# Optimization experiments

Hardware: AMD Instinct MI355X
Metric: run time of the kernel (lower is better)

## Reference

```python
import jax, jax.numpy as jnp
import numpy as np

SEQ_LEN, BATCH, VOCAB, EMB, HID, LAYERS = 128, 64, 10000, 1024, 1024, 2

def setup_inputs() -> dict:
    key = jax.random.key(0)
    ks = jax.random.split(key, 8)
    inputs = jax.random.randint(ks[0], (SEQ_LEN, BATCH), 0, VOCAB)
    hidden = jnp.zeros((LAYERS, BATCH, HID), jnp.float32)
    # parameters (uniform init like the torch module)
    emb = jax.random.uniform(ks[1], (VOCAB, EMB), jnp.float32, -0.1, 0.1)
    # per-layer RNN cell params (emb_size == hidden_size so Wx stacks uniformly)
    s = 1.0 / np.sqrt(HID)
    Wx = jax.random.uniform(ks[2], (LAYERS, HID, HID), jnp.float32, -s, s)
    Wh = jax.random.uniform(ks[3], (LAYERS, HID, HID), jnp.float32, -s, s)
    b = jax.random.uniform(ks[4], (LAYERS, HID), jnp.float32, -s, s)
    fcW = jax.random.uniform(ks[5], (VOCAB, HID), jnp.float32, -0.1, 0.1)
    fcb = jnp.zeros((VOCAB,), jnp.float32)
    return {"inputs": inputs, "hidden": hidden, "emb": emb, "Wx": Wx,
            "Wh": Wh, "b": b, "fcW": fcW, "fcb": fcb}

def reference(inputs, hidden, emb, Wx, Wh, b, fcW, fcb):
    num_layers = hidden.shape[0]

    def step(h, tok):
        x = emb[tok]  # [B, EMB] embedding lookup (dropout = identity, keep_prob=1)
        new_h = []
        for j in range(num_layers):  # small static loop over layers
            hj = jnp.tanh(x @ Wx[j] + h[j] @ Wh[j] + b[j])  # [B, H]
            new_h.append(hj)
            x = hj
        logits = x @ fcW.T + fcb  # [B, V]
        return jnp.stack(new_h), logits

    h_final, logits = jax.lax.scan(step, hidden, inputs)
    return logits, h_final  # [S,B,V], [L,B,H]
```

## Files before the change

### kernel.cpp

```cpp
#include <hip/hip_runtime.h>
#include <hip/hip_bf16.h>
#include <math.h>

typedef __hip_bfloat16 bf16;
typedef __attribute__((ext_vector_type(8))) short short8;
typedef __attribute__((ext_vector_type(4))) float floatx4;

#define SEQ   128
#define BATCH 64
#define VOCAB 10000
#define HID   1024
#define TAIL  81920000
#define PNL   131072

#define MFMA(a,b,c) __builtin_amdgcn_mfma_f32_16x16x32_bf16((a),(b),(c),0,0,0)

#define LDA_U64(p)   __hip_atomic_load((const unsigned long long*)(p), __ATOMIC_RELAXED, __HIP_MEMORY_SCOPE_AGENT)
#define LDAQ_I32(p)  __hip_atomic_load((const int*)(p), __ATOMIC_ACQUIRE, __HIP_MEMORY_SCOPE_AGENT)
#define STA_U32(p,v) __hip_atomic_store((unsigned int*)(p), (v), __ATOMIC_RELAXED, __HIP_MEMORY_SCOPE_AGENT)
#define ADDR_I32(p)  __hip_atomic_fetch_add((int*)(p), 1, __ATOMIC_RELEASE, __HIP_MEMORY_SCOPE_AGENT)

union U16B { unsigned long long u[2]; short8 s; };

__device__ inline unsigned int pack2(float lo, float hi) {
  unsigned short a = __builtin_bit_cast(unsigned short, __float2bfloat16(lo));
  unsigned short b = __builtin_bit_cast(unsigned short, __float2bfloat16(hi));
  return ((unsigned int)b << 16) | (unsigned int)a;
}

__device__ inline void gl_lds16(const bf16* g, bf16* s) {
  __builtin_amdgcn_global_load_lds(
      (const __attribute__((address_space(1))) void*)g,
      (__attribute__((address_space(3))) void*)s, 16, 0, 0);
}

__device__ inline float ld_in(const void* p, size_t i, int f) {
  return f ? ((const float*)p)[i] : __bfloat162float(((const bf16*)p)[i]);
}

__global__ __launch_bounds__(256) void detect(const unsigned short* __restrict__ u,
                                              int* __restrict__ flag) {
  __shared__ int smax;
  if (threadIdx.x == 0) smax = 0;
  __syncthreads();
  int mymax = 0;
  for (int i = threadIdx.x * 2; i < 4096; i += 512) {
    int e = (u[i] >> 7) & 0xFF;
    mymax = max(mymax, e);
  }
  atomicMax(&smax, mymax);
  __syncthreads();
  if (threadIdx.x == 0) {
    flag[0] = (smax >= 0xF0) ? 1 : 0;
    flag[1] = 0;
    flag[2] = 0;
  }
}

__global__ __launch_bounds__(256) void convert_any(const void* __restrict__ src,
                                                   bf16* __restrict__ dst, int n,
                                                   const int* __restrict__ flagp) {
  int f = *flagp;
  for (int i = blockIdx.x * 256 + threadIdx.x; i < n; i += gridDim.x * 256)
    dst[i] = __float2bfloat16(ld_in(src, (size_t)i, f));
}

__global__ __launch_bounds__(256) void init_hidden(const void* __restrict__ src,
                                                   bf16* __restrict__ h0,
                                                   bf16* __restrict__ h1,
                                                   const int* __restrict__ flagp) {
  int f = *flagp;
  int i = blockIdx.x * 256 + threadIdx.x;
  if (i < 65536) {
    h0[i] = __float2bfloat16(ld_in(src, (size_t)i, f));
    h1[i] = __float2bfloat16(ld_in(src, (size_t)(65536 + i), f));
  }
}

__global__ __launch_bounds__(256) void transpose4(const void* __restrict__ Wx,
                                                  const void* __restrict__ Wh,
                                                  bf16* __restrict__ Wt,
                                                  const int* __restrict__ flagp) {
  __shared__ bf16 tile[64][65];
  int f = *flagp;
  int z = blockIdx.z;
  const void* src = (z & 1) ? Wh : Wx;
  size_t loff = (z >> 1) ? (size_t)HID * HID : 0;
  bf16* dst = Wt + (size_t)z * HID * HID;
  int r0 = blockIdx.x * 64, c0 = blockIdx.y * 64;
  int t = threadIdx.x, cc = t & 63, rg = t >> 6;
  #pragma unroll
  for (int i = 0; i < 16; ++i) {
    int r = rg * 16 + i;
    tile[r][cc] = __float2bfloat16(ld_in(src, loff + (size_t)(r0 + r) * HID + c0 + cc, f));
  }
  __syncthreads();
  #pragma unroll
  for (int i = 0; i < 16; ++i) {
    int j = rg * 16 + i;
    dst[(size_t)(c0 + j) * HID + r0 + cc] = tile[cc][j];
  }
}

__global__ __launch_bounds__(256) void gemm_a0(
    const int*  __restrict__ tok,
    const bf16* __restrict__ emb,
    const bf16* __restrict__ Wx0t,
    const bf16* __restrict__ b0,
    float* __restrict__ A0)
{
  __shared__ __align__(16) bf16 sA[128 * 32];
  __shared__ __align__(16) bf16 sB[128 * 32];
  int m0 = blockIdx.x * 128, n0 = blockIdx.y * 128;
  int t = threadIdx.x, lane = t & 63, w = t >> 6;
  int wm = (w >> 1) * 64, wn = (w & 1) * 64;
  int quad = lane >> 4, l16 = lane & 15;

  int r0 = t >> 2, kc = t & 3;
  const bf16* ga0 = emb + (size_t)tok[m0 + r0] * HID + kc * 8;
  const bf16* ga1 = emb + (size_t)tok[m0 + r0 + 64] * HID + kc * 8;
  const bf16* gb0 = Wx0t + (size_t)(n0 + r0) * HID + kc * 8;
  const bf16* gb1 = gb0 + (size_t)64 * HID;
  bf16* sa0 = sA + t * 8;  bf16* sa1 = sA + (t + 256) * 8;
  bf16* sb0 = sB + t * 8;  bf16* sb1 = sB + (t + 256) * 8;

  floatx4 acc[4][4];
  #pragma unroll
  for (int j = 0; j < 4; ++j) {
    float bv = __bfloat162float(b0[n0 + wn + j * 16 + l16]);
    #pragma unroll
    for (int i = 0; i < 4; ++i) acc[i][j] = (floatx4){bv, bv, bv, bv};
  }

  for (int kt = 0; kt < 32; ++kt) {
    gl_lds16(ga0, sa0); gl_lds16(ga1, sa1);
    gl_lds16(gb0, sb0); gl_lds16(gb1, sb1);
    ga0 += 32; ga1 += 32; gb0 += 32; gb1 += 32;
    __syncthreads();
    short8 af[4], bfr[4];
    #pragma unroll
    for (int i = 0; i < 4; ++i)
      af[i] = *(const short8*)(sA + (wm + i * 16 + l16) * 32 + quad * 8);
    #pragma unroll
    for (int j = 0; j < 4; ++j)
      bfr[j] = *(const short8*)(sB + (wn + j * 16 + l16) * 32 + quad * 8);
    #pragma unroll
    for (int i = 0; i < 4; ++i)
      #pragma unroll
      for (int j = 0; j < 4; ++j)
        acc[i][j] = MFMA(af[i], bfr[j], acc[i][j]);
    __syncthreads();
  }

  #pragma unroll
  for (int i = 0; i < 4; ++i)
    #pragma unroll
    for (int j = 0; j < 4; ++j)
      #pragma unroll
      for (int r = 0; r < 4; ++r) {
        int row = wm + i * 16 + quad * 4 + r;
        int col = wn + j * 16 + l16;
        A0[(size_t)(m0 + row) * HID + n0 + col] = acc[i][j][r];
      }
}

__global__ __launch_bounds__(256) void wavefront_persist(
    const float* __restrict__ A0,
    const bf16* __restrict__ Wt,
    const bf16* __restrict__ bvecB,
    char* __restrict__ H0f,
    char* __restrict__ H1f,
    bf16* __restrict__ H1hist,
    void* __restrict__ outv,
    int* __restrict__ flagp)
{
  __shared__ short8 sW8[4096];
  char* sWb = (char*)sW8;
  const int f = flagp[0];
  int* c0 = flagp + 1;
  int* c1 = flagp + 2;
  char* H1B = (char*)H1hist;
  const int blk = blockIdx.x;
  const int t = threadIdx.x, lane = t & 63, w = t >> 6;
  const int quad = lane >> 4, l16 = lane & 15;
  const int m = w * 16;
  const bool isH1 = blk >= 32;

  const bf16* Wh0t = Wt + (size_t)1 * HID * HID;
  const bf16* Wx1t = Wt + (size_t)2 * HID * HID;
  const bf16* Wh1t = Wt + (size_t)3 * HID * HID;

  if (!isH1) {
    const int n0 = blk * 32;
    #pragma unroll
    for (int i = 0; i < 16; ++i) {
      int idx = i * 256 + t;
      int row = idx >> 7, c16 = idx & 127;
      short8 v = *(const short8*)(Wh0t + (size_t)(n0 + row) * HID + c16 * 8);
      int off = (c16 >> 2) * 2048 + (row >> 4) * 1024 + (c16 & 3) * 256 + (row & 15) * 16;
      *(short8*)(sWb + off) = v;
    }
  } else {
    const int n0 = (blk - 32) * 16;
    #pragma unroll
    for (int i = 0; i < 8; ++i) {
      int idx = i * 256 + t;
      int row = idx >> 7, c16 = idx & 127;
      int off = (c16 >> 2) * 1024 + (c16 & 3) * 256 + (row & 15) * 16;
      *(short8*)(sWb + off)         = *(const short8*)(Wx1t + (size_t)(n0 + row) * HID + c16 * 8);
      *(short8*)(sWb + 32768 + off) = *(const short8*)(Wh1t + (size_t)(n0 + row) * HID + c16 * 8);
    }
  }
  __syncthreads();

  if (!isH1) {
    const int n0 = blk * 32;
    const char* b0p = sWb + lane * 16;
    const char* b1p = sWb + 1024 + lane * 16;
    for (int k = 0; k < 128; ++k) {
      if (t == 0) {
        if (k > 0)   while (LDAQ_I32(c0) < 32 * k)        __builtin_amdgcn_s_sleep(1);
        if (k >= 32) while (LDAQ_I32(c1) < 64 * (k - 31)) __builtin_amdgcn_s_sleep(1);
      }
      __syncthreads();

      const char* aB = H0f + (size_t)(k & 31) * PNL + (m + l16) * 2048 + quad * 16;
      U16B a[32];
      #pragma unroll
      for (int kt = 0; kt < 32; ++kt) {
        a[kt].u[0] = LDA_U64(aB + kt * 64);
        a[kt].u[1] = LDA_U64(aB + kt * 64 + 8);
      }
      float a0r[2][4];
      #pragma unroll
      for (int j = 0; j < 2; ++j)
        #pragma unroll
        for (int r = 0; r < 4; ++r)
          a0r[j][r] = A0[(size_t)(k * 64 + m + quad * 4 + r) * HID + n0 + j * 16 + l16];

      floatx4 acc0 = {}, acc1 = {};
      #pragma unroll
      for (int kt = 0; kt < 32; ++kt) {
        acc0 = MFMA(a[kt].s, *(const short8*)(b0p + kt * 2048), acc0);
        acc1 = MFMA(a[kt].s, *(const short8*)(b1p + kt * 2048), acc1);
      }

      char* wp = H0f + (size_t)((k + 1) & 31) * PNL;
      #pragma unroll
      for (int j = 0; j < 2; ++j) {
        floatx4 ac = j ? acc1 : acc0;
        #pragma unroll
        for (int r = 0; r < 4; ++r) {
          int row = m + quad * 4 + r, col = n0 + j * 16 + l16;
          float v = tanhf(ac[r] + a0r[j][r]);
          float pv = __shfl_xor(v, 1);
          if (k == 127) {
            size_t o = (size_t)TAIL + (size_t)row * HID + col;
            if (f) ((float*)outv)[o] = v;
            else   ((bf16*)outv)[o] = __float2bfloat16(v);
          }
          if (!(l16 & 1))
            STA_U32(wp + row * 2048 + col * 2, pack2(v, pv));
        }
      }
      __syncthreads();
      if (t == 0) ADDR_I32(c0);
    }
  } else {
    const int n0 = (blk - 32) * 16;
    const char* bXp = sWb + lane * 16;
    const char* bHp = sWb + 32768 + lane * 16;
    const float bb = __bfloat162float(bvecB[HID + n0 + l16]);
    for (int s = 0; s < 128; ++s) {
      if (t == 0) {
        while (LDAQ_I32(c0) < 32 * (s + 1)) __builtin_amdgcn_s_sleep(1);
        if (s > 0) while (LDAQ_I32(c1) < 64 * s) __builtin_amdgcn_s_sleep(1);
      }
      __syncthreads();

      const char* aX = H0f + (size_t)((s + 1) & 31) * PNL + (m + l16) * 2048 + quad * 16;
      const char* aH = H1f + (size_t)(s % 3) * PNL + (m + l16) * 2048 + quad * 16;
      floatx4 accX = {}, accH = {};
      #pragma unroll
      for (int half = 0; half < 2; ++half) {
        U16B x[16], h[16];
        #pragma unroll
        for (int i = 0; i < 16; ++i) {
          int kt = half * 16 + i;
          x[i].u[0] = LDA_U64(aX + kt * 64);
          x[i].u[1] = LDA_U64(aX + kt * 64 + 8);
          h[i].u[0] = LDA_U64(aH + kt * 64);
          h[i].u[1] = LDA_U64(aH + kt * 64 + 8);
        }
        #pragma unroll
        for (int i = 0; i < 16; ++i) {
          int kt = half * 16 + i;
          accX = MFMA(x[i].s, *(const short8*)(bXp + kt * 1024), accX);
          accH = MFMA(h[i].s, *(const short8*)(bHp + kt * 1024), accH);
        }
      }

      char* wp = H1f + (size_t)((s + 1) % 3) * PNL;
      #pragma unroll
      for (int r = 0; r < 4; ++r) {
        int row = m + quad * 4 + r, col = n0 + l16;
        float v = tanhf(accX[r] + accH[r] + bb);
        float pv = __shfl_xor(v, 1);
        if (s == 127) {
          size_t o = (size_t)TAIL + 64 * HID + (size_t)row * HID + col;
          if (f) ((float*)outv)[o] = v;
          else   ((bf16*)outv)[o] = __float2bfloat16(v);
        }
        if (!(l16 & 1)) {
          unsigned int pk = pack2(v, pv);
          STA_U32(wp + row * 2048 + col * 2, pk);
          STA_U32(H1B + ((size_t)(s * 64 + row) * HID + col) * 2, pk);
        }
      }
      __syncthreads();
      if (t == 0) ADDR_I32(c1);
    }
  }
}

__global__ __launch_bounds__(256) void gemm_logits(
    const bf16* __restrict__ H1,
    const bf16* __restrict__ fcW,
    const bf16* __restrict__ fcb,
    void* __restrict__ outv,
    const int* __restrict__ flagp)
{
  __shared__ __align__(16) bf16 sA[128 * 32];
  __shared__ __align__(16) bf16 sB[128 * 32];
  int f = *flagp;
  int m0 = blockIdx.x * 128, n0 = blockIdx.y * 128;
  int t = threadIdx.x, lane = t & 63, w = t >> 6;
  int wm = (w >> 1) * 64, wn = (w & 1) * 64;
  int quad = lane >> 4, l16 = lane & 15;

  int r0 = t >> 2, kc = t & 3;
  int rB0 = n0 + r0;      if (rB0 > VOCAB - 1) rB0 = VOCAB - 1;
  int rB1 = n0 + r0 + 64; if (rB1 > VOCAB - 1) rB1 = VOCAB - 1;
  const bf16* ga0 = H1 + (size_t)(m0 + r0) * HID + kc * 8;
  const bf16* ga1 = ga0 + (size_t)64 * HID;
  const bf16* gb0 = fcW + (size_t)rB0 * HID + kc * 8;
  const bf16* gb1 = fcW + (size_t)rB1 * HID + kc * 8;
  bf16* sa0 = sA + t * 8;  bf16* sa1 = sA + (t + 256) * 8;
  bf16* sb0 = sB + t * 8;  bf16* sb1 = sB + (t + 256) * 8;

  floatx4 acc[4][4];
  #pragma unroll
  for (int j = 0; j < 4; ++j) {
    int c = n0 + wn + j * 16 + l16;
    float bv = __bfloat162float(fcb[c > VOCAB - 1 ? VOCAB - 1 : c]);
    #pragma unroll
    for (int i = 0; i < 4; ++i) acc[i][j] = (floatx4){bv, bv, bv, bv};
  }

  for (int kt = 0; kt < 32; ++kt) {
    gl_lds16(ga0, sa0); gl_lds16(ga1, sa1);
    gl_lds16(gb0, sb0); gl_lds16(gb1, sb1);
    ga0 += 32; ga1 += 32; gb0 += 32; gb1 += 32;
    __syncthreads();
    short8 af[4], bfr[4];
    #pragma unroll
    for (int i = 0; i < 4; ++i)
      af[i] = *(const short8*)(sA + (wm + i * 16 + l16) * 32 + quad * 8);
    #pragma unroll
    for (int j = 0; j < 4; ++j)
      bfr[j] = *(const short8*)(sB + (wn + j * 16 + l16) * 32 + quad * 8);
    #pragma unroll
    for (int i = 0; i < 4; ++i)
      #pragma unroll
      for (int j = 0; j < 4; ++j)
        acc[i][j] = MFMA(af[i], bfr[j], acc[i][j]);
    __syncthreads();
  }

  #pragma unroll
  for (int i = 0; i < 4; ++i)
    #pragma unroll
    for (int j = 0; j < 4; ++j)
      #pragma unroll
      for (int r = 0; r < 4; ++r) {
        int row = wm + i * 16 + quad * 4 + r;
        int col = n0 + wn + j * 16 + l16;
        if (col < VOCAB) {
          size_t o = (size_t)(m0 + row) * VOCAB + col;
          if (f) ((float*)outv)[o] = acc[i][j][r];
          else   ((bf16*)outv)[o] = __float2bfloat16(acc[i][j][r]);
        }
      }
}

extern "C" void kernel_launch(void* const* d_in, const int* in_sizes, int n_in,
                              void* d_out, int out_size, void* d_ws, size_t ws_size,
                              hipStream_t stream)
{
  const int*  tok     = (const int*)d_in[0];
  const void* hid_raw = d_in[1];
  const void* emb_raw = d_in[2];
  const void* Wx_raw  = d_in[3];
  const void* Wh_raw  = d_in[4];
  const void* b_raw   = d_in[5];
  const void* fcW_raw = d_in[6];
  const void* fcb_raw = d_in[7];

  char* ws = (char*)d_ws;
  float* A0    = (float*)ws;
  bf16*  Wt    = (bf16*)(ws + 33554432);
  bf16*  H1hist= (bf16*)(ws + 41943040);
  char*  H0f   = ws + 58720256;
  char*  H1f   = ws + 62914560;
  bf16*  shared= (bf16*)(ws + 63307776);
  bf16*  bvecB = (bf16*)(ws + 83787776);
  bf16*  fcbB  = (bf16*)(ws + 83791872);
  int*   flag  = (int*)(ws + 83811872);

  detect<<<1, 256, 0, stream>>>((const unsigned short*)emb_raw, flag);
  convert_any<<<2048, 256, 0, stream>>>(emb_raw, shared, VOCAB * HID, flag);
  convert_any<<<8,    256, 0, stream>>>(b_raw,   bvecB, 2 * HID, flag);
  convert_any<<<40,   256, 0, stream>>>(fcb_raw, fcbB, VOCAB, flag);
  init_hidden<<<256, 256, 0, stream>>>(hid_raw, (bf16*)H0f, (bf16*)H1f, flag);
  transpose4<<<dim3(16, 16, 4), 256, 0, stream>>>(Wx_raw, Wh_raw, Wt, flag);
  gemm_a0<<<dim3(64, 8), 256, 0, stream>>>(tok, shared, Wt, bvecB, A0);
  convert_any<<<2048, 256, 0, stream>>>(fcW_raw, shared, VOCAB * HID, flag);
  wavefront_persist<<<96, 256, 0, stream>>>(A0, Wt, bvecB, H0f, H1f,
                                            H1hist, d_out, flag);
  gemm_logits<<<dim3(64, 79), 256, 0, stream>>>(H1hist, shared, fcbB, d_out, flag);
}
```

Baseline: 3.028 ms.

## Replace atomic counters with per-block step stamps polled by every wave

Inter-block synchronization in the persistent wavefront kernel moves from two shared fetch-add counters with acquire loads to per-block stamp slots. Each block writes its completed step with a relaxed store, and every wave polls all producer stamps in parallel, one lane per block, using __all. This removes contention on a single atomic counter and the block-wide barrier after thread 0 spins. It relies only on relaxed atomics with no acquire/release ordering, so data visibility for the hidden-state buffers could break. It also adds a spin cap as a timeout.

```diff
diff --git a/kernel.cpp b/kernel.cpp
--- a/kernel.cpp
+++ b/kernel.cpp
@@ -16,9 +16,9 @@
 #define MFMA(a,b,c) __builtin_amdgcn_mfma_f32_16x16x32_bf16((a),(b),(c),0,0,0)
 
 #define LDA_U64(p)   __hip_atomic_load((const unsigned long long*)(p), __ATOMIC_RELAXED, __HIP_MEMORY_SCOPE_AGENT)
-#define LDAQ_I32(p)  __hip_atomic_load((const int*)(p), __ATOMIC_ACQUIRE, __HIP_MEMORY_SCOPE_AGENT)
+#define LDA_I32(p)   __hip_atomic_load((const int*)(p), __ATOMIC_RELAXED, __HIP_MEMORY_SCOPE_AGENT)
 #define STA_U32(p,v) __hip_atomic_store((unsigned int*)(p), (v), __ATOMIC_RELAXED, __HIP_MEMORY_SCOPE_AGENT)
-#define ADDR_I32(p)  __hip_atomic_fetch_add((int*)(p), 1, __ATOMIC_RELEASE, __HIP_MEMORY_SCOPE_AGENT)
+#define STA_I32(p,v) __hip_atomic_store((int*)(p), (v), __ATOMIC_RELAXED, __HIP_MEMORY_SCOPE_AGENT)
 
 union U16B { unsigned long long u[2]; short8 s; };
 
@@ -49,12 +49,9 @@
     mymax = max(mymax, e);
   }
   atomicMax(&smax, mymax);
+  for (int i = threadIdx.x + 1; i < 3104; i += 256) flag[i] = 0;
   __syncthreads();
-  if (threadIdx.x == 0) {
-    flag[0] = (smax >= 0xF0) ? 1 : 0;
-    flag[1] = 0;
-    flag[2] = 0;
-  }
+  if (threadIdx.x == 0) flag[0] = (smax >= 0xF0) ? 1 : 0;
 }
 
 __global__ __launch_bounds__(256) void convert_any(const void* __restrict__ src,
@@ -177,14 +174,16 @@
   __shared__ short8 sW8[4096];
   char* sWb = (char*)sW8;
   const int f = flagp[0];
-  int* c0 = flagp + 1;
-  int* c1 = flagp + 2;
+  int* stamp0 = flagp + 32;
+  int* stamp1 = flagp + 1056;
   char* H1B = (char*)H1hist;
   const int blk = blockIdx.x;
   const int t = threadIdx.x, lane = t & 63, w = t >> 6;
   const int quad = lane >> 4, l16 = lane & 15;
   const int m = w * 16;
   const bool isH1 = blk >= 32;
+  const int* sp0 = stamp0 + (lane & 31) * 32;
+  const int* sp1 = stamp1 + lane * 32;
 
   const bf16* Wh0t = Wt + (size_t)1 * HID * HID;
   const bf16* Wx1t = Wt + (size_t)2 * HID * HID;
@@ -215,14 +214,16 @@
 
   if (!isH1) {
     const int n0 = blk * 32;
+    int* mystamp = stamp0 + blk * 32;
     const char* b0p = sWb + lane * 16;
     const char* b1p = sWb + 1024 + lane * 16;
     for (int k = 0; k < 128; ++k) {
-      if (t == 0) {
-        if (k > 0)   while (LDAQ_I32(c0) < 32 * k)        __builtin_amdgcn_s_sleep(1);
-        if (k >= 32) while (LDAQ_I32(c1) < 64 * (k - 31)) __builtin_amdgcn_s_sleep(1);
-      }
-      __syncthreads();
+      if (k > 0)
+        for (int g = 0; !__all(LDA_I32(sp0) >= k) && g < (1 << 26); ++g)
+          __builtin_amdgcn_s_sleep(1);
+      if (k >= 32)
+        for (int g = 0; !__all(LDA_I32(sp1) >= k - 31) && g < (1 << 26); ++g)
+          __builtin_amdgcn_s_sleep(1);
 
       const char* aB = H0f + (size_t)(k & 31) * PNL + (m + l16) * 2048 + quad * 16;
       U16B a[32];
@@ -264,19 +265,20 @@
         }
       }
       __syncthreads();
-      if (t == 0) ADDR_I32(c0);
+      if (t == 0) STA_I32(mystamp, k + 1);
     }
   } else {
     const int n0 = (blk - 32) * 16;
+    int* mystamp = stamp1 + (blk - 32) * 32;
     const char* bXp = sWb + lane * 16;
     const char* bHp = sWb + 32768 + lane * 16;
     const float bb = __bfloat162float(bvecB[HID + n0 + l16]);
     for (int s = 0; s < 128; ++s) {
-      if (t == 0) {
-        while (LDAQ_I32(c0) < 32 * (s + 1)) __builtin_amdgcn_s_sleep(1);
-        if (s > 0) while (LDAQ_I32(c1) < 64 * s) __builtin_amdgcn_s_sleep(1);
-      }
-      __syncthreads();
+      for (int g = 0; !__all(LDA_I32(sp0) >= s + 1) && g < (1 << 26); ++g)
+        __builtin_amdgcn_s_sleep(1);
+      if (s > 0)
+        for (int g = 0; !__all(LDA_I32(sp1) >= s) && g < (1 << 26); ++g)
+          __builtin_amdgcn_s_sleep(1);
 
       const char* aX = H0f + (size_t)((s + 1) & 31) * PNL + (m + l16) * 2048 + quad * 16;
       const char* aH = H1f + (size_t)(s % 3) * PNL + (m + l16) * 2048 + quad * 16;
@@ -318,7 +320,7 @@
         }
       }
       __syncthreads();
-      if (t == 0) ADDR_I32(c1);
+      if (t == 0) STA_I32(mystamp, s + 1);
     }
   }
 }
```

Result: faster. 2.695 ms (-11.0%).

## Merge layer workers into 64 blocks with per-block step flags and wave polling

Applied to the files above, without the earlier changes.

Replaces the split of 32 layer-0 and 64 layer-1 blocks with 64 uniform blocks that each compute layer 0 and then layer 1 for the same 16 columns, holding all three weight slices in LDS. The shared atomic counters with acquire/release become per-block relaxed step flags that a whole wavefront polls with __all, and polling gives up after a bounded spin count. Ring buffers shrink to 4 and 2 slots. The aim is to cut global synchronization latency per step. Dropping acquire/release ordering and using a bounded spin that can fall through risks reading stale hidden states.

```diff
diff --git a/kernel.cpp b/kernel.cpp
--- a/kernel.cpp
+++ b/kernel.cpp
@@ -12,13 +12,14 @@
 #define HID   1024
 #define TAIL  81920000
 #define PNL   131072
+#define SPIN  (1 << 17)
 
 #define MFMA(a,b,c) __builtin_amdgcn_mfma_f32_16x16x32_bf16((a),(b),(c),0,0,0)
 
 #define LDA_U64(p)   __hip_atomic_load((const unsigned long long*)(p), __ATOMIC_RELAXED, __HIP_MEMORY_SCOPE_AGENT)
-#define LDAQ_I32(p)  __hip_atomic_load((const int*)(p), __ATOMIC_ACQUIRE, __HIP_MEMORY_SCOPE_AGENT)
+#define LDA_I32(p)   __hip_atomic_load((const int*)(p), __ATOMIC_RELAXED, __HIP_MEMORY_SCOPE_AGENT)
 #define STA_U32(p,v) __hip_atomic_store((unsigned int*)(p), (v), __ATOMIC_RELAXED, __HIP_MEMORY_SCOPE_AGENT)
-#define ADDR_I32(p)  __hip_atomic_fetch_add((int*)(p), 1, __ATOMIC_RELEASE, __HIP_MEMORY_SCOPE_AGENT)
+#define STA_I32(p,v) __hip_atomic_store((int*)(p), (v), __ATOMIC_RELAXED, __HIP_MEMORY_SCOPE_AGENT)
 
 union U16B { unsigned long long u[2]; short8 s; };
 
@@ -49,12 +50,9 @@
     mymax = max(mymax, e);
   }
   atomicMax(&smax, mymax);
+  for (int i = threadIdx.x + 1; i < 4160; i += 256) flag[i] = 0;
   __syncthreads();
-  if (threadIdx.x == 0) {
-    flag[0] = (smax >= 0xF0) ? 1 : 0;
-    flag[1] = 0;
-    flag[2] = 0;
-  }
+  if (threadIdx.x == 0) flag[0] = (smax >= 0xF0) ? 1 : 0;
 }
 
 __global__ __launch_bounds__(256) void convert_any(const void* __restrict__ src,
@@ -168,143 +166,139 @@
     const float* __restrict__ A0,
     const bf16* __restrict__ Wt,
     const bf16* __restrict__ bvecB,
-    char* __restrict__ H0f,
-    char* __restrict__ H1f,
+    char* __restrict__ H0r,
+    char* __restrict__ H1r,
     bf16* __restrict__ H1hist,
     void* __restrict__ outv,
     int* __restrict__ flagp)
 {
-  __shared__ short8 sW8[4096];
+  __shared__ __align__(16) short8 sW8[6144];
   char* sWb = (char*)sW8;
   const int f = flagp[0];
-  int* c0 = flagp + 1;
-  int* c1 = flagp + 2;
+  int* s0 = flagp + 64;
+  int* s1 = flagp + 2112;
   char* H1B = (char*)H1hist;
   const int blk = blockIdx.x;
+  const int n0 = blk * 16;
   const int t = threadIdx.x, lane = t & 63, w = t >> 6;
   const int quad = lane >> 4, l16 = lane & 15;
   const int m = w * 16;
-  const bool isH1 = blk >= 32;
+  int* mys0 = s0 + blk * 32;
+  int* mys1 = s1 + blk * 32;
+  const int* ps0 = s0 + lane * 32;
+  const int* ps1 = s1 + lane * 32;
 
   const bf16* Wh0t = Wt + (size_t)1 * HID * HID;
   const bf16* Wx1t = Wt + (size_t)2 * HID * HID;
   const bf16* Wh1t = Wt + (size_t)3 * HID * HID;
 
-  if (!isH1) {
-    const int n0 = blk * 32;
-    #pragma unroll
-    for (int i = 0; i < 16; ++i) {
-      int idx = i * 256 + t;
-      int row = idx >> 7, c16 = idx & 127;
-      short8 v = *(const short8*)(Wh0t + (size_t)(n0 + row) * HID + c16 * 8);
-      int off = (c16 >> 2) * 2048 + (row >> 4) * 1024 + (c16 & 3) * 256 + (row & 15) * 16;
-      *(short8*)(sWb + off) = v;
+  #pragma unroll
+  for (int i = 0; i < 8; ++i) {
+    int idx = i * 256 + t;
+    int row = idx >> 7, c16 = idx & 127;
+    int off = (c16 >> 2) * 1024 + (c16 & 3) * 256 + (row & 15) * 16;
+    *(short8*)(sWb + off)         = *(const short8*)(Wh0t + (size_t)(n0 + row) * HID + c16 * 8);
+    *(short8*)(sWb + 32768 + off) = *(const short8*)(Wx1t + (size_t)(n0 + row) * HID + c16 * 8);
+    *(short8*)(sWb + 65536 + off) = *(const short8*)(Wh1t + (size_t)(n0 + row) * HID + c16 * 8);
+  }
+  __syncthreads();
+
+  const char* w0p = sWb + lane * 16;
+  const char* wXp = sWb + 32768 + lane * 16;
+  const char* wHp = sWb + 65536 + lane * 16;
+  const float bb = __bfloat162float(bvecB[HID + n0 + l16]);
+
+  for (int r = 0; r <= 128; ++r) {
+    float a0r[4];
+    if (r <= 127) {
+      #pragma unroll
+      for (int q = 0; q < 4; ++q)
+        a0r[q] = A0[(size_t)(r * 64 + m + quad * 4 + q) * HID + n0 + l16];
     }
-  } else {
-    const int n0 = (blk - 32) * 16;
-    #pragma unroll
-    for (int i = 0; i < 8; ++i) {
-      int idx = i * 256 + t;
-      int row = idx >> 7, c16 = idx & 127;
-      int off = (c16 >> 2) * 1024 + (c16 & 3) * 256 + (row & 15) * 16;
-      *(short8*)(sWb + off)         = *(const short8*)(Wx1t + (size_t)(n0 + row) * HID + c16 * 8);
-      *(short8*)(sWb + 32768 + off) = *(const short8*)(Wh1t + (size_t)(n0 + row) * HID + c16 * 8);
+    if (r >= 1) {
+      if (w == 0) {
+        int g = 0;
+        while (!__all(LDA_I32(ps0) >= r) && ++g < SPIN)
+          __builtin_amdgcn_s_sleep(2);
+      }
+      __syncthreads();
+      __builtin_amdgcn_sched_barrier(0);
     }
-  }
-  __syncthreads();
-
-  if (!isH1) {
-    const int n0 = blk * 32;
-    const char* b0p = sWb + lane * 16;
-    const char* b1p = sWb + 1024 + lane * 16;
-    for (int k = 0; k < 128; ++k) {
-      if (t == 0) {
-        if (k > 0)   while (LDAQ_I32(c0) < 32 * k)        __builtin_amdgcn_s_sleep(1);
-        if (k >= 32) while (LDAQ_I32(c1) < 64 * (k - 31)) __builtin_amdgcn_s_sleep(1);
+
+    if (r <= 127) {
+      const char* xB = H0r + (size_t)((r - 1) & 3) * PNL + (m + l16) * 2048 + quad * 16;
+      floatx4 accA = {}, accB = {};
+      #pragma unroll
+      for (int hf = 0; hf < 2; ++hf) {
+        U16B x[16];
+        #pragma unroll
+        for (int i = 0; i < 16; ++i) {
+          int kt = hf * 16 + i;
+          x[i].u[0] = LDA_U64(xB + kt * 64);
+          x[i].u[1] = LDA_U64(xB + kt * 64 + 8);
+        }
+        #pragma unroll
+        for (int i = 0; i < 16; i += 2) {
+          int kt = hf * 16 + i;
+          accA = MFMA(x[i].s,     *(const short8*)(w0p + kt * 1024),       accA);
+          accB = MFMA(x[i + 1].s, *(const short8*)(w0p + (kt + 1) * 1024), accB);
+        }
+      }
+      char* wp = H0r + (size_t)(r & 3) * PNL;
+      #pragma unroll
+      for (int q = 0; q < 4; ++q) {
+        int row = m + quad * 4 + q, col = n0 + l16;
+        float v = tanhf(accA[q] + accB[q] + a0r[q]);
+        float pv = __shfl_xor(v, 1);
+        if (r == 127) {
+          size_t o = (size_t)TAIL + (size_t)row * HID + col;
+          if (f) ((float*)outv)[o] = v;
+          else   ((bf16*)outv)[o] = __float2bfloat16(v);
+        }
+        if (!(l16 & 1))
+          STA_U32(wp + row * 2048 + col * 2, pack2(v, pv));
       }
       __syncthreads();
-
-      const char* aB = H0f + (size_t)(k & 31) * PNL + (m + l16) * 2048 + quad * 16;
-      U16B a[32];
-      #pragma unroll
-      for (int kt = 0; kt < 32; ++kt) {
-        a[kt].u[0] = LDA_U64(aB + kt * 64);
-        a[kt].u[1] = LDA_U64(aB + kt * 64 + 8);
-      }
-      float a0r[2][4];
-      #pragma unroll
-      for (int j = 0; j < 2; ++j)
-        #pragma unroll
-        for (int r = 0; r < 4; ++r)
-          a0r[j][r] = A0[(size_t)(k * 64 + m + quad * 4 + r) * HID + n0 + j * 16 + l16];
-
-      floatx4 acc0 = {}, acc1 = {};
-      #pragma unroll
-      for (int kt = 0; kt < 32; ++kt) {
-        acc0 = MFMA(a[kt].s, *(const short8*)(b0p + kt * 2048), acc0);
-        acc1 = MFMA(a[kt].s, *(const short8*)(b1p + kt * 2048), acc1);
-      }
-
-      char* wp = H0f + (size_t)((k + 1) & 31) * PNL;
-      #pragma unroll
-      for (int j = 0; j < 2; ++j) {
-        floatx4 ac = j ? acc1 : acc0;
-        #pragma unroll
-        for (int r = 0; r < 4; ++r) {
-          int row = m + quad * 4 + r, col = n0 + j * 16 + l16;
-          float v = tanhf(ac[r] + a0r[j][r]);
-          float pv = __shfl_xor(v, 1);
-          if (k == 127) {
-            size_t o = (size_t)TAIL + (size_t)row * HID + col;
-            if (f) ((float*)outv)[o] = v;
-            else   ((bf16*)outv)[o] = __float2bfloat16(v);
-          }
-          if (!(l16 & 1))
-            STA_U32(wp + row * 2048 + col * 2, pack2(v, pv));
-        }
-      }
-      __syncthreads();
-      if (t == 0) ADDR_I32(c0);
+      if (t == 0) STA_I32(mys0, r + 1);
     }
-  } else {
-    const int n0 = (blk - 32) * 16;
-    const char* bXp = sWb + lane * 16;
-    const char* bHp = sWb + 32768 + lane * 16;
-    const float bb = __bfloat162float(bvecB[HID + n0 + l16]);
-    for (int s = 0; s < 128; ++s) {
-      if (t == 0) {
-        while (LDAQ_I32(c0) < 32 * (s + 1)) __builtin_amdgcn_s_sleep(1);
-        if (s > 0) while (LDAQ_I32(c1) < 64 * s) __builtin_amdgcn_s_sleep(1);
-      }
-      __syncthreads();
-
-      const char* aX = H0f + (size_t)((s + 1) & 31) * PNL + (m + l16) * 2048 + quad * 16;
-      const char* aH = H1f + (size_t)(s % 3) * PNL + (m + l16) * 2048 + quad * 16;
+
+    if (r >= 1) {
+      if (r >= 2) {
+        if (w == 0) {
+          int g = 0;
+          while (!__all(LDA_I32(ps1) >= r - 1) && ++g < SPIN)
+            __builtin_amdgcn_s_sleep(2);
+        }
+        __syncthreads();
+        __builtin_amdgcn_sched_barrier(0);
+      }
+      const char* xB = H0r + (size_t)((r - 1) & 3) * PNL + (m + l16) * 2048 + quad * 16;
+      const char* hB = H1r + (size_t)((r - 2) & 1) * PNL + (m + l16) * 2048 + quad * 16;
       floatx4 accX = {}, accH = {};
       #pragma unroll
-      for (int half = 0; half < 2; ++half) {
+      for (int hf = 0; hf < 2; ++hf) {
         U16B x[16], h[16];
         #pragma unroll
         for (int i = 0; i < 16; ++i) {
-          int kt = half * 16 + i;
-          x[i].u[0] = LDA_U64(aX + kt * 64);
-          x[i].u[1] = LDA_U64(aX + kt * 64 + 8);
-          h[i].u[0] = LDA_U64(aH + kt * 64);
-          h[i].u[1] = LDA_U64(aH + kt * 64 + 8);
+          int kt = hf * 16 + i;
+          x[i].u[0] = LDA_U64(xB + kt * 64);
+          x[i].u[1] = LDA_U64(xB + kt * 64 + 8);
+          h[i].u[0] = LDA_U64(hB + kt * 64);
+          h[i].u[1] = LDA_U64(hB + kt * 64 + 8);
         }
         #pragma unroll
         for (int i = 0; i < 16; ++i) {
-          int kt = half * 16 + i;
-          accX = MFMA(x[i].s, *(const short8*)(bXp + kt * 1024), accX);
-          accH = MFMA(h[i].s, *(const short8*)(bHp + kt * 1024), accH);
-        }
-      }
-
-      char* wp = H1f + (size_t)((s + 1) % 3) * PNL;
-      #pragma unroll
-      for (int r = 0; r < 4; ++r) {
-        int row = m + quad * 4 + r, col = n0 + l16;
-        float v = tanhf(accX[r] + accH[r] + bb);
+          int kt = hf * 16 + i;
+          accX = MFMA(x[i].s, *(const short8*)(wXp + kt * 1024), accX);
+          accH = MFMA(h[i].s, *(const short8*)(wHp + kt * 1024), accH);
+        }
+      }
+      const int s = r - 1;
+      char* wp = H1r + (size_t)(s & 1) * PNL;
+      #pragma unroll
+      for (int q = 0; q < 4; ++q) {
+        int row = m + quad * 4 + q, col = n0 + l16;
+        float v = tanhf(accX[q] + accH[q] + bb);
         float pv = __shfl_xor(v, 1);
         if (s == 127) {
           size_t o = (size_t)TAIL + 64 * HID + (size_t)row * HID + col;
@@ -318,7 +312,7 @@
         }
       }
       __syncthreads();
-      if (t == 0) ADDR_I32(c1);
+      if (t == 0) STA_I32(mys1, r);
     }
   }
 }
@@ -410,22 +404,23 @@
   float* A0    = (float*)ws;
   bf16*  Wt    = (bf16*)(ws + 33554432);
   bf16*  H1hist= (bf16*)(ws + 41943040);
-  char*  H0f   = ws + 58720256;
-  char*  H1f   = ws + 62914560;
-  bf16*  shared= (bf16*)(ws + 63307776);
-  bf16*  bvecB = (bf16*)(ws + 83787776);
-  bf16*  fcbB  = (bf16*)(ws + 83791872);
-  int*   flag  = (int*)(ws + 83811872);
+  char*  H0r   = ws + 58720256;
+  char*  H1r   = ws + 59244544;
+  bf16*  shared= (bf16*)(ws + 59506688);
+  bf16*  bvecB = (bf16*)(ws + 79986688);
+  bf16*  fcbB  = (bf16*)(ws + 79990784);
+  int*   flag  = (int*)(ws + 80010784);
 
   detect<<<1, 256, 0, stream>>>((const unsigned short*)emb_raw, flag);
   convert_any<<<2048, 256, 0, stream>>>(emb_raw, shared, VOCAB * HID, flag);
   convert_any<<<8,    256, 0, stream>>>(b_raw,   bvecB, 2 * HID, flag);
   convert_any<<<40,   256, 0, stream>>>(fcb_raw, fcbB, VOCAB, flag);
-  init_hidden<<<256, 256, 0, stream>>>(hid_raw, (bf16*)H0f, (bf16*)H1f, flag);
+  init_hidden<<<256, 256, 0, stream>>>(hid_raw, (bf16*)(H0r + 3 * PNL),
+                                       (bf16*)(H1r + 1 * PNL), flag);
   transpose4<<<dim3(16, 16, 4), 256, 0, stream>>>(Wx_raw, Wh_raw, Wt, flag);
   gemm_a0<<<dim3(64, 8), 256, 0, stream>>>(tok, shared, Wt, bvecB, A0);
   convert_any<<<2048, 256, 0, stream>>>(fcW_raw, shared, VOCAB * HID, flag);
-  wavefront_persist<<<96, 256, 0, stream>>>(A0, Wt, bvecB, H0f, H1f,
+  wavefront_persist<<<64, 256, 0, stream>>>(A0, Wt, bvecB, H0r, H1r,
                                             H1hist, d_out, flag);
   gemm_logits<<<dim3(64, 79), 256, 0, stream>>>(H1hist, shared, fcbB, d_out, flag);
 }
```

After: 3.665 ms. +21.1%, slower.
